# Optimization experiments

Measured on AMD Instinct MI355X. Metric: run time of the kernel, lower is better.

## Reference

```python
import jax, jax.numpy as jnp
import numpy as np

N = 50000; E = 600000; D = 128; NB = 20; L = 3; H = 64; NG = 512; ZMAX = 100
CUTOFF = 5.0

def setup_inputs() -> dict:
    key = jax.random.key(0)
    ks = jax.random.split(key, 32)
    inp = {}
    inp['at_no'] = jax.random.randint(ks[0], (N,), 0, ZMAX)
    inp['pos'] = jax.random.normal(ks[1], (N, 3), dtype=jnp.float32) * 3.0
    inp['edge_index'] = jax.random.randint(ks[2], (2, E), 0, N)
    inp['batch'] = jnp.sort(jax.random.randint(ks[3], (N,), 0, NG))
    def w(k, shape, fan_in):
        return (jax.random.normal(k, shape, dtype=jnp.float32) / np.sqrt(fan_in)).astype(jnp.float32)
    inp['emb'] = w(ks[4], (ZMAX, D), 1.0)
    # per-block filter net: rbf -> 3D
    inp['Wf'] = w(ks[5], (L, NB, 3 * D), NB); inp['bf'] = jnp.zeros((L, 3 * D), jnp.float32)
    # per-block message scalar MLP: D -> D -> 3D
    inp['Wm1'] = w(ks[6], (L, D, D), D);      inp['bm1'] = jnp.zeros((L, D), jnp.float32)
    inp['Wm2'] = w(ks[7], (L, D, 3 * D), D);  inp['bm2'] = jnp.zeros((L, 3 * D), jnp.float32)
    # per-block update: U, V channel-mixing on vectors; MLP 2D -> D -> 3D
    inp['U'] = w(ks[8], (L, D, D), D)
    inp['V'] = w(ks[9], (L, D, D), D)
    inp['Wu1'] = w(ks[10], (L, 2 * D, D), 2 * D); inp['bu1'] = jnp.zeros((L, D), jnp.float32)
    inp['Wu2'] = w(ks[11], (L, D, 3 * D), D);     inp['bu2'] = jnp.zeros((L, 3 * D), jnp.float32)
    # scalar output head: D -> H -> 1, graph sum
    inp['Wo1'] = w(ks[12], (D, H), D); inp['bo1'] = jnp.zeros((H,), jnp.float32)
    inp['Wo2'] = w(ks[13], (H, 1), H); inp['bo2'] = jnp.zeros((1,), jnp.float32)
    return inp

def _painn(at_no, pos, edge_index, batch, emb, Wf, bf, Wm1, bm1, Wm2, bm2,
           U, V, Wu1, bu1, Wu2, bu2, Wo1, bo1, Wo2, bo2):
    src, dst = edge_index[0], edge_index[1]
    vec = pos[dst] - pos[src]                       # [E,3]
    dist = jnp.sqrt(jnp.sum(vec * vec, axis=-1, keepdims=True) + 1e-12)  # [E,1]
    dirv = vec / dist                               # [E,3] (rsh l=1)
    n = jnp.arange(1, NB + 1, dtype=jnp.float32)
    rbf = jnp.sin(n * jnp.pi * dist / CUTOFF) / dist            # [E,NB] Bessel
    fcut = 0.5 * (jnp.cos(jnp.pi * dist / CUTOFF) + 1.0) * (dist < CUTOFF)  # [E,1]

    x = emb[at_no]                                  # [N,D]
    v = jnp.zeros((x.shape[0], 3, D), x.dtype)      # [N,3,D]

    for l in range(L):
        # ---- message ----
        filt = (rbf @ Wf[l] + bf[l]) * fcut                     # [E,3D]
        phi = jax.nn.silu(x @ Wm1[l] + bm1[l]) @ Wm2[l] + bm2[l]  # [N,3D]
        m = phi[src] * filt                                     # [E,3D]
        ds, dv1, dv2 = m[:, :D], m[:, D:2 * D], m[:, 2 * D:]
        dv = dv1[:, None, :] * dirv[:, :, None] + dv2[:, None, :] * v[src]  # [E,3,D]
        x = x + jax.ops.segment_sum(ds, dst, num_segments=N)
        v = v + jax.ops.segment_sum(dv, dst, num_segments=N)
        # ---- update ----
        Uv = jnp.einsum('ncd,de->nce', v, U[l])
        Vv = jnp.einsum('ncd,de->nce', v, V[l])
        Vn = jnp.sqrt(jnp.sum(Vv * Vv, axis=1) + 1e-8)          # [N,D]
        a = jax.nn.silu(jnp.concatenate([x, Vn], axis=-1) @ Wu1[l] + bu1[l]) @ Wu2[l] + bu2[l]
        avv, asv, ass = a[:, :D], a[:, D:2 * D], a[:, 2 * D:]
        x = x + ass + asv * jnp.sum(Uv * Vv, axis=1)
        v = v + avv[:, None, :] * Uv

    node_out = jax.nn.silu(x @ Wo1 + bo1) @ Wo2 + bo2           # [N,1]
    return jax.ops.segment_sum(node_out, batch, num_segments=NG)  # [NG,1]

def reference(at_no, pos, edge_index, batch, emb, Wf, bf, Wm1, bm1, Wm2, bm2,
              U, V, Wu1, bu1, Wu2, bu2, Wo1, bo1, Wo2, bo2):
    return _painn(at_no, pos, edge_index, batch, emb, Wf, bf, Wm1, bm1, Wm2, bm2,
                  U, V, Wu1, bu1, Wu2, bu2, Wo1, bo1, Wo2, bo2)
```

## Files before the change

kernel.cpp:

```cpp
#include <hip/hip_runtime.h>
#include <math.h>

#define NN 50000
#define NE 600000
#define ECAP 230000
#define DD 128
#define D3 384
#define NB_ 20
#define HH 64
#define NG_ 512
#define LSZ 180224

typedef short v8s __attribute__((ext_vector_type(8)));
typedef short v4sh __attribute__((ext_vector_type(4)));
typedef float v4f __attribute__((ext_vector_type(4)));

__device__ __forceinline__ float silu_f(float z) { return z / (1.0f + expf(-z)); }

__device__ __forceinline__ short f2bf(float f) {
  unsigned u = __float_as_uint(f);
  u += 0x7FFF + ((u >> 16) & 1);
  return (short)(u >> 16);
}
__device__ __forceinline__ float bf2f(short s) {
  return __uint_as_float(((unsigned)(unsigned short)s) << 16);
}
__device__ __forceinline__ void split2(float x, short& h, short& l) {
  h = f2bf(x);
  l = f2bf(x - bf2f(h));
}
#define SPLIT8(f0, f1, ah, al) { short h,l; \
  split2(f0.x,h,l); ah[0]=h; al[0]=l;  split2(f0.y,h,l); ah[1]=h; al[1]=l; \
  split2(f0.z,h,l); ah[2]=h; al[2]=l;  split2(f0.w,h,l); ah[3]=h; al[3]=l; \
  split2(f1.x,h,l); ah[4]=h; al[4]=l;  split2(f1.y,h,l); ah[5]=h; al[5]=l; \
  split2(f1.z,h,l); ah[6]=h; al[6]=l;  split2(f1.w,h,l); ah[7]=h; al[7]=l; }
__device__ __forceinline__ void split_store4(float4 f, short* hp, short* lp) {
  short h0,l0,h1,l1,h2,l2,h3,l3;
  split2(f.x,h0,l0); split2(f.y,h1,l1); split2(f.z,h2,l2); split2(f.w,h3,l3);
  v4sh hv = {h0,h1,h2,h3}, lv = {l0,l1,l2,l3};
  *(v4sh*)hp = hv; *(v4sh*)lp = lv;
}
#define MFMA3(acc, ah, al, bh, bl) \
  acc = __builtin_amdgcn_mfma_f32_16x16x32_bf16(ah, bh, acc, 0, 0, 0); \
  acc = __builtin_amdgcn_mfma_f32_16x16x32_bf16(al, bh, acc, 0, 0, 0); \
  acc = __builtin_amdgcn_mfma_f32_16x16x32_bf16(ah, bl, acc, 0, 0, 0);

__global__ void zero_f_kernel(float* __restrict__ p, long n) {
  long i = (long)blockIdx.x * blockDim.x + threadIdx.x;
  long s = (long)gridDim.x * blockDim.x;
  for (; i < n; i += s) p[i] = 0.0f;
}

__global__ void zero_i_kernel(int* __restrict__ p, long n) {
  long i = (long)blockIdx.x * blockDim.x + threadIdx.x;
  long s = (long)gridDim.x * blockDim.x;
  for (; i < n; i += s) p[i] = 0;
}

__global__ void init_x_kernel(const int* __restrict__ at_no, const float* __restrict__ emb,
                              float* __restrict__ x) {
  int i = blockIdx.x * blockDim.x + threadIdx.x;
  if (i >= NN * DD) return;
  x[i] = emb[at_no[i >> 7] * DD + (i & 127)];
}

__global__ void prep_w_kernel(const float* __restrict__ Wm1, const float* __restrict__ Wm2,
                              const float* __restrict__ U, const float* __restrict__ V,
                              const float* __restrict__ Wu1, const float* __restrict__ Wu2,
                              short* __restrict__ hi, short* __restrict__ lo) {
  int idx = blockIdx.x * 256 + threadIdx.x;
  if (idx >= 3 * LSZ) return;
  int l = idx / LSZ, r = idx % LSZ;
  const float* src; int K, N, nk;
  if (r < 16384)       { src = Wm1 + (size_t)l*16384; K = 128; N = 128; nk = r; }
  else if (r < 65536)  { src = Wm2 + (size_t)l*49152; K = 128; N = 384; nk = r - 16384; }
  else if (r < 81920)  { src = U   + (size_t)l*16384; K = 128; N = 128; nk = r - 65536; }
  else if (r < 98304)  { src = V   + (size_t)l*16384; K = 128; N = 128; nk = r - 81920; }
  else if (r < 131072) { src = Wu1 + (size_t)l*32768; K = 256; N = 128; nk = r - 98304; }
  else                 { src = Wu2 + (size_t)l*49152; K = 128; N = 384; nk = r - 131072; }
  int n = nk / K, k = nk - n * K;
  float xx = src[(size_t)k * N + n];
  short h = f2bf(xx);
  hi[idx] = h;
  lo[idx] = f2bf(xx - bf2f(h));
}

__global__ void hist_kernel(const int* __restrict__ ei, const float* __restrict__ pos,
                            int* __restrict__ counts) {
  int e = blockIdx.x * blockDim.x + threadIdx.x;
  if (e >= NE) return;
  int s = ei[e], d = ei[NE + e];
  float dx = pos[3*d]   - pos[3*s];
  float dy = pos[3*d+1] - pos[3*s+1];
  float dz = pos[3*d+2] - pos[3*s+2];
  float d2 = dx*dx + dy*dy + dz*dz + 1e-12f;
  if (d2 < 25.0f) atomicAdd(&counts[d], 1);
}

__global__ void scan_kernel(const int* __restrict__ counts, int* __restrict__ indptr, int n) {
  __shared__ int sm[1024];
  __shared__ int carry_s;
  if (threadIdx.x == 0) carry_s = 0;
  __syncthreads();
  for (int start = 0; start < n; start += 1024) {
    int i = start + (int)threadIdx.x;
    int val = (i < n) ? counts[i] : 0;
    sm[threadIdx.x] = val;
    __syncthreads();
    for (int off = 1; off < 1024; off <<= 1) {
      int t = (threadIdx.x >= (unsigned)off) ? sm[threadIdx.x - off] : 0;
      __syncthreads();
      sm[threadIdx.x] += t;
      __syncthreads();
    }
    int c = carry_s;
    if (i < n) indptr[i] = c + sm[threadIdx.x] - val;
    __syncthreads();
    if (threadIdx.x == 0) carry_s = c + sm[1023];
    __syncthreads();
  }
  if (threadIdx.x == 0) indptr[n] = carry_s;
}

__global__ void fill_kernel(const int* __restrict__ ei, const float* __restrict__ pos,
                            const int* __restrict__ indptr, int* __restrict__ cursor,
                            int* __restrict__ srcs, float4* __restrict__ eg1,
                            float4* __restrict__ eg2) {
  int e = blockIdx.x * blockDim.x + threadIdx.x;
  if (e >= NE) return;
  int s = ei[e], d = ei[NE + e];
  float dx = pos[3*d]   - pos[3*s];
  float dy = pos[3*d+1] - pos[3*s+1];
  float dz = pos[3*d+2] - pos[3*s+2];
  float d2 = dx*dx + dy*dy + dz*dz + 1e-12f;
  if (d2 < 25.0f) {
    int p = atomicAdd(&cursor[d], 1);
    int slot = indptr[d] + p;
    float dist = sqrtf(d2);
    float inv = 1.0f / dist;
    float wang = 0.62831853071795864769f * dist;
    float s1 = __sinf(wang), c1 = __cosf(wang);
    float fc = 0.5f * (c1 + 1.0f);
    srcs[slot] = s;
    eg1[slot] = make_float4(s1, c1, fc, fc * inv);
    eg2[slot] = make_float4(dx * inv, dy * inv, dz * inv, 0.0f);
  }
}

template<bool SILU>
__global__ void __launch_bounds__(256) mfma_gemm_kernel(
    const float* A, const short* __restrict__ Bth, const short* __restrict__ Btl,
    const float* __restrict__ bias, float* C, int M) {
  __shared__ short As2[2 * 32 * 136];
  #define ASH(r,c) As2[(r)*136 + (c)]
  #define ASL(r,c) As2[4352 + (r)*136 + (c)]
  int tid = threadIdx.x;
  long r0 = (long)blockIdx.x * 32;
  #pragma unroll
  for (int i = 0; i < 4; i++) {
    int lin = i*256 + tid;
    int r = lin >> 5, c4 = lin & 31;
    long row = r0 + r; if (row >= M) row = M - 1;
    float4 f = *(const float4*)(A + row*128 + c4*4);
    split_store4(f, &ASH(r, c4*4), &ASL(r, c4*4));
  }
  __syncthreads();
  int lane = tid & 63, wv = tid >> 6;
  int l15 = lane & 15, q = lane >> 4;
  v4f acc[2][2] = {};
  #pragma unroll
  for (int s = 0; s < 4; s++) {
    v8s ah[2], al[2];
    #pragma unroll
    for (int mt = 0; mt < 2; mt++) {
      ah[mt] = *(const v8s*)&ASH(mt*16 + l15, s*32 + q*8);
      al[mt] = *(const v8s*)&ASL(mt*16 + l15, s*32 + q*8);
    }
    #pragma unroll
    for (int nt = 0; nt < 2; nt++) {
      int n = (2*wv + nt)*16 + l15;
      v8s bh = *(const v8s*)(Bth + (long)n*128 + s*32 + q*8);
      v8s bl = *(const v8s*)(Btl + (long)n*128 + s*32 + q*8);
      #pragma unroll
      for (int mt = 0; mt < 2; mt++) { MFMA3(acc[mt][nt], ah[mt], al[mt], bh, bl); }
    }
  }
  #pragma unroll
  for (int nt = 0; nt < 2; nt++) {
    int n = (2*wv + nt)*16 + l15;
    float bb = bias[n];
    #pragma unroll
    for (int mt = 0; mt < 2; mt++)
      #pragma unroll
      for (int i = 0; i < 4; i++) {
        long row = r0 + mt*16 + q*4 + i;
        if (row < M) {
          float val = acc[mt][nt][i] + bb;
          if constexpr (SILU) val = silu_f(val);
          C[row*128 + n] = val;
        }
      }
  }
  #undef ASH
  #undef ASL
}

__global__ void __launch_bounds__(512) mfma_gemm_phi_kernel(
    const float* A, const short* __restrict__ Bth, const short* __restrict__ Btl,
    const float* __restrict__ bias,
    float* __restrict__ C0, float* __restrict__ C1, float* C2, int M) {
  __shared__ short As2[2 * 32 * 136];
  #define ASH(r,c) As2[(r)*136 + (c)]
  #define ASL(r,c) As2[4352 + (r)*136 + (c)]
  int tid = threadIdx.x;
  long r0 = (long)blockIdx.x * 32;
  #pragma unroll
  for (int i = 0; i < 2; i++) {
    int lin = i*512 + tid;
    int r = lin >> 5, c4 = lin & 31;
    long row = r0 + r; if (row >= M) row = M - 1;
    float4 f = *(const float4*)(A + row*128 + c4*4);
    split_store4(f, &ASH(r, c4*4), &ASL(r, c4*4));
  }
  __syncthreads();
  int lane = tid & 63, wv = tid >> 6;
  int l15 = lane & 15, q = lane >> 4;
  v4f acc[2][3] = {};
  #pragma unroll
  for (int s = 0; s < 4; s++) {
    v8s ah[2], al[2];
    #pragma unroll
    for (int mt = 0; mt < 2; mt++) {
      ah[mt] = *(const v8s*)&ASH(mt*16 + l15, s*32 + q*8);
      al[mt] = *(const v8s*)&ASL(mt*16 + l15, s*32 + q*8);
    }
    #pragma unroll
    for (int j = 0; j < 3; j++) {
      int n = (wv*3 + j)*16 + l15;
      v8s bh = *(const v8s*)(Bth + (long)n*128 + s*32 + q*8);
      v8s bl = *(const v8s*)(Btl + (long)n*128 + s*32 + q*8);
      #pragma unroll
      for (int mt = 0; mt < 2; mt++) { MFMA3(acc[mt][j], ah[mt], al[mt], bh, bl); }
    }
  }
  #pragma unroll
  for (int j = 0; j < 3; j++) {
    int n = (wv*3 + j)*16 + l15;
    int sl = n >> 7, col = n & 127;
    float* C = (sl == 0) ? C0 : (sl == 1) ? C1 : C2;
    float bb = bias[n];
    #pragma unroll
    for (int mt = 0; mt < 2; mt++)
      #pragma unroll
      for (int i = 0; i < 4; i++) {
        long row = r0 + mt*16 + q*4 + i;
        if (row < M) C[row*128 + col] = acc[mt][j][i] + bb;
      }
  }
  #undef ASH
  #undef ASL
}

__global__ void __launch_bounds__(512) muva_kernel(
    const float* __restrict__ phi0, const float* __restrict__ phi1,
    const float* __restrict__ phi2, const float* __restrict__ vA,
    float* __restrict__ vB, float* __restrict__ x,
    const int* __restrict__ srcs, const float4* __restrict__ eg1,
    const float4* __restrict__ eg2, const int* __restrict__ indptr,
    const float* __restrict__ Wf_l, const float* __restrict__ bf_l,
    const short* __restrict__ Uth, const short* __restrict__ Utl,
    const short* __restrict__ Vth, const short* __restrict__ Vtl,
    const short* __restrict__ W1h, const short* __restrict__ W1l, const float* __restrict__ b1,
    const short* __restrict__ W2h, const short* __restrict__ W2l, const float* __restrict__ b2) {
  __shared__ float smem[8704];
  #define VN(r,c)  smem[(r)*136 + (c)]
  #define XN(r,c)  smem[6528 + (r)*136 + (c)]
  #define CAT(r,c) smem[(r)*272 + (c)]
  #define T2(r,c)  smem[4352 + (r)*136 + (c)]
  const long NND = (long)NN*DD;
  int tid = threadIdx.x;
  long nb = (long)blockIdx.x * 16;
  {
    int g = tid >> 7, d = tid & 127;
    float wf0[NB_], wf1[NB_], wf2[NB_];
    #pragma unroll
    for (int k = 0; k < NB_; k++) {
      wf0[k] = Wf_l[k*D3 + d];
      wf1[k] = Wf_l[k*D3 + DD + d];
      wf2[k] = Wf_l[k*D3 + 2*DD + d];
    }
    float bf0 = bf_l[d], bf1 = bf_l[DD + d], bf2 = bf_l[2*DD + d];
    for (int j = 0; j < 4; j++) {
      int nr = 4*g + j;
      long n = nb + nr;
      int t = indptr[n], end = indptr[n+1];
      float xacc = 0.f, a0 = 0.f, a1 = 0.f, a2 = 0.f;
      float4 g1C = {}, g2C = {};
      float p0C = 0.f, p1C = 0.f, p2C = 0.f, w0C = 0.f, w1C = 0.f, w2C = 0.f;
      if (t < end) {
        int s0 = srcs[t]; g1C = eg1[t]; g2C = eg2[t];
        long b = (long)s0*DD + d;
        p0C = phi0[b]; p1C = phi1[b]; p2C = phi2[b];
        w0C = vA[b]; w1C = vA[NND + b]; w2C = vA[2*NND + b];
      }
      for (; t < end; t++) {
        float4 gg = g1C, dv = g2C;
        float p0 = p0C, p1 = p1C, p2 = p2C, w0 = w0C, w1 = w1C, w2 = w2C;
        if (t + 1 < end) {
          int sN = srcs[t+1]; g1C = eg1[t+1]; g2C = eg2[t+1];
          long b = (long)sN*DD + d;
          p0C = phi0[b]; p1C = phi1[b]; p2C = phi2[b];
          w0C = vA[b]; w1C = vA[NND + b]; w2C = vA[2*NND + b];
        }
        float c2 = 2.0f * gg.y;
        float rkm1 = 0.f, rk = gg.x, dot0 = 0.f, dot1 = 0.f, dot2 = 0.f;
        #pragma unroll
        for (int k = 0; k < NB_; k++) {
          dot0 = fmaf(rk, wf0[k], dot0);
          dot1 = fmaf(rk, wf1[k], dot1);
          dot2 = fmaf(rk, wf2[k], dot2);
          float rn = fmaf(c2, rk, -rkm1);
          rkm1 = rk; rk = rn;
        }
        xacc = fmaf(p0, bf0*gg.z + gg.w*dot0, xacc);
        float m1 = p1 * (bf1*gg.z + gg.w*dot1);
        float m2 = p2 * (bf2*gg.z + gg.w*dot2);
        a0 = fmaf(m1, dv.x, fmaf(m2, w0, a0));
        a1 = fmaf(m1, dv.y, fmaf(m2, w1, a1));
        a2 = fmaf(m1, dv.z, fmaf(m2, w2, a2));
      }
      long b = n*DD + d;
      XN(nr, d) = x[b] + xacc;
      VN(nr, d)      = vA[b]         + a0;
      VN(16 + nr, d) = vA[NND + b]   + a1;
      VN(32 + nr, d) = vA[2*NND + b] + a2;
    }
  }
  __syncthreads();
  int lane = tid & 63, wv = tid >> 6;
  int l15 = lane & 15, q = lane >> 4;
  int d = wv*16 + l15;
  v4f aU[3] = {}, aV[3] = {};
  #pragma unroll
  for (int s = 0; s < 4; s++) {
    long boff = (long)d*128 + s*32 + q*8;
    v8s buh = *(const v8s*)(Uth + boff);
    v8s bul = *(const v8s*)(Utl + boff);
    v8s bvh = *(const v8s*)(Vth + boff);
    v8s bvl = *(const v8s*)(Vtl + boff);
    #pragma unroll
    for (int c = 0; c < 3; c++) {
      float4 f0 = *(const float4*)&VN(c*16 + l15, s*32 + q*8);
      float4 f1 = *(const float4*)&VN(c*16 + l15, s*32 + q*8 + 4);
      v8s ah, al;
      SPLIT8(f0, f1, ah, al);
      MFMA3(aU[c], ah, al, buh, bul);
      MFMA3(aV[c], ah, al, bvh, bvl);
    }
  }
  float sreg[4], vn2[4];
  #pragma unroll
  for (int i = 0; i < 4; i++) {
    sreg[i] = aU[0][i]*aV[0][i] + aU[1][i]*aV[1][i] + aU[2][i]*aV[2][i];
    vn2[i]  = aV[0][i]*aV[0][i] + aV[1][i]*aV[1][i] + aV[2][i]*aV[2][i];
  }
  float vold[4][3];
  #pragma unroll
  for (int i = 0; i < 4; i++)
    #pragma unroll
    for (int c = 0; c < 3; c++) vold[i][c] = VN(c*16 + q*4 + i, d);
  __syncthreads();
  {
    int r = tid >> 5, c4 = tid & 31;
    *(float4*)&CAT(r, c4*4) = *(const float4*)&XN(r, c4*4);
  }
  #pragma unroll
  for (int i = 0; i < 4; i++)
    CAT(q*4 + i, 128 + d) = sqrtf(vn2[i] + 1e-8f);
  __syncthreads();
  {
    v4f acc = {};
    #pragma unroll
    for (int s = 0; s < 8; s++) {
      float4 f0 = *(const float4*)&CAT(l15, s*32 + q*8);
      float4 f1 = *(const float4*)&CAT(l15, s*32 + q*8 + 4);
      v8s ah, al;
      SPLIT8(f0, f1, ah, al);
      v8s bh = *(const v8s*)(W1h + (long)d*256 + s*32 + q*8);
      v8s bl = *(const v8s*)(W1l + (long)d*256 + s*32 + q*8);
      MFMA3(acc, ah, al, bh, bl);
    }
    float bb = b1[d];
    #pragma unroll
    for (int i = 0; i < 4; i++)
      T2(q*4 + i, d) = silu_f(acc[i] + bb);
  }
  __syncthreads();
  {
    v4f acc[3] = {};
    #pragma unroll
    for (int s = 0; s < 4; s++) {
      float4 f0 = *(const float4*)&T2(l15, s*32 + q*8);
      float4 f1 = *(const float4*)&T2(l15, s*32 + q*8 + 4);
      v8s ah, al;
      SPLIT8(f0, f1, ah, al);
      #pragma unroll
      for (int g = 0; g < 3; g++) {
        int n = g*128 + d;
        v8s bh = *(const v8s*)(W2h + (long)n*128 + s*32 + q*8);
        v8s bl = *(const v8s*)(W2l + (long)n*128 + s*32 + q*8);
        MFMA3(acc[g], ah, al, bh, bl);
      }
    }
    float bavv = b2[d], basv = b2[128 + d], bass = b2[256 + d];
    #pragma unroll
    for (int i = 0; i < 4; i++) {
      int lr = q*4 + i;
      long row = nb + lr;
      float avv = acc[0][i] + bavv;
      float asv = acc[1][i] + basv;
      float ass = acc[2][i] + bass;
      x[row*DD + d] = CAT(lr, d) + ass + asv * sreg[i];
      #pragma unroll
      for (int c = 0; c < 3; c++)
        vB[(long)c*NND + row*DD + d] = fmaf(avv, aU[c][i], vold[i][c]);
    }
  }
  #undef VN
  #undef XN
  #undef CAT
  #undef T2
}

__global__ void __launch_bounds__(256) out_kernel(
    const float* __restrict__ x, const float* __restrict__ Wo1,
    const float* __restrict__ bo1, const float* __restrict__ Wo2,
    const float* __restrict__ bo2, const int* __restrict__ batch,
    float* __restrict__ out) {
  __shared__ float xs[4][132];
  int tid = threadIdx.x;
  long n0 = (long)blockIdx.x * 4;
  if (tid < 128) {
    int r = tid >> 5, c4 = tid & 31;
    *(float4*)&xs[r][c4*4] = *(const float4*)(x + (n0 + r)*128 + c4*4);
  }
  __syncthreads();
  int wv = tid >> 6, t = tid & 63;
  float acc = bo1[t];
  #pragma unroll 16
  for (int k = 0; k < DD; k++) acc = fmaf(xs[wv][k], Wo1[k*HH + t], acc);
  float val = silu_f(acc) * Wo2[t];
  #pragma unroll
  for (int off = 32; off > 0; off >>= 1) val += __shfl_down(val, off);
  if (t == 0) atomicAdd(&out[batch[n0 + wv]], val + bo2[0]);
}

extern "C" void kernel_launch(void* const* d_in, const int* in_sizes, int n_in,
                              void* d_out, int out_size, void* d_ws, size_t ws_size,
                              hipStream_t stream) {
  const int*   at_no = (const int*)d_in[0];
  const float* pos   = (const float*)d_in[1];
  const int*   ei    = (const int*)d_in[2];
  const int*   batch = (const int*)d_in[3];
  const float* emb   = (const float*)d_in[4];
  const float* Wf    = (const float*)d_in[5];
  const float* bfp   = (const float*)d_in[6];
  const float* Wm1   = (const float*)d_in[7];
  const float* bm1   = (const float*)d_in[8];
  const float* Wm2   = (const float*)d_in[9];
  const float* bm2   = (const float*)d_in[10];
  const float* U     = (const float*)d_in[11];
  const float* V     = (const float*)d_in[12];
  const float* Wu1   = (const float*)d_in[13];
  const float* bu1   = (const float*)d_in[14];
  const float* Wu2   = (const float*)d_in[15];
  const float* bu2   = (const float*)d_in[16];
  const float* Wo1   = (const float*)d_in[17];
  const float* bo1   = (const float*)d_in[18];
  const float* Wo2   = (const float*)d_in[19];
  const float* bo2   = (const float*)d_in[20];
  float* out = (float*)d_out;

  char* w = (char*)d_ws;
  auto alloc = [&](size_t bytes) -> void* {
    void* p = (void*)w;
    w += (bytes + 255) & ~(size_t)255;
    return p;
  };
  float*  x      = (float*)alloc(sizeof(float)*(size_t)NN*DD);
  float*  v_a    = (float*)alloc(sizeof(float)*(size_t)NN*D3);
  float*  v_b    = (float*)alloc(sizeof(float)*(size_t)NN*D3);
  float*  t1     = (float*)alloc(sizeof(float)*(size_t)NN*DD);
  float*  phiS   = (float*)alloc(sizeof(float)*(size_t)NN*DD);
  float*  phi0   = (float*)alloc(sizeof(float)*(size_t)NN*DD);
  short*  wbh    = (short*)alloc(sizeof(short)*(size_t)3*LSZ);
  short*  wbl    = (short*)alloc(sizeof(short)*(size_t)3*LSZ);
  int*    srcs   = (int*)alloc(sizeof(int)*(size_t)ECAP);
  float4* eg1    = (float4*)alloc(sizeof(float4)*(size_t)ECAP);
  float4* eg2    = (float4*)alloc(sizeof(float4)*(size_t)ECAP);
  int*    indptr = (int*)alloc(sizeof(int)*((size_t)NN+1));
  int*    counts = (int*)alloc(sizeof(int)*(size_t)NN);

  if ((size_t)(w - (char*)d_ws) > ws_size) {
    zero_f_kernel<<<2, 256, 0, stream>>>(out, NG_);
    return;
  }

  zero_f_kernel<<<2048, 256, 0, stream>>>(v_a, (long)NN*D3);
  zero_f_kernel<<<2, 256, 0, stream>>>(out, NG_);
  zero_i_kernel<<<64, 256, 0, stream>>>(counts, NN);
  init_x_kernel<<<(NN*DD + 255)/256, 256, 0, stream>>>(at_no, emb, x);
  prep_w_kernel<<<(3*LSZ + 255)/256, 256, 0, stream>>>(Wm1, Wm2, U, V, Wu1, Wu2, wbh, wbl);
  hist_kernel<<<(NE + 255)/256, 256, 0, stream>>>(ei, pos, counts);
  scan_kernel<<<1, 1024, 0, stream>>>(counts, indptr, NN);
  zero_i_kernel<<<64, 256, 0, stream>>>(counts, NN);
  fill_kernel<<<(NE + 255)/256, 256, 0, stream>>>(ei, pos, indptr, counts, srcs, eg1, eg2);

  const int MB = (NN + 31) / 32;
  float* vcur = v_a;
  float* vnext = v_b;
  for (int l = 0; l < 3; l++) {
    const float* Wf_l  = Wf  + (size_t)l*NB_*D3;
    const float* bf_l  = bfp + (size_t)l*D3;
    const float* bm1_l = bm1 + (size_t)l*DD;
    const float* bm2_l = bm2 + (size_t)l*D3;
    const float* bu1_l = bu1 + (size_t)l*DD;
    const float* bu2_l = bu2 + (size_t)l*D3;
    const short* Lh = wbh + (size_t)l*LSZ;
    const short* Ll = wbl + (size_t)l*LSZ;
    const short* Wm1h = Lh,          *Wm1L = Ll;
    const short* Wm2h = Lh + 16384,  *Wm2L = Ll + 16384;
    const short* Uh   = Lh + 65536,  *UL   = Ll + 65536;
    const short* Vh   = Lh + 81920,  *VL   = Ll + 81920;
    const short* Wu1h = Lh + 98304,  *Wu1L = Ll + 98304;
    const short* Wu2h = Lh + 131072, *Wu2L = Ll + 131072;

    mfma_gemm_kernel<true><<<MB, 256, 0, stream>>>(x, Wm1h, Wm1L, bm1_l, t1, NN);
    mfma_gemm_phi_kernel<<<MB, 512, 0, stream>>>(t1, Wm2h, Wm2L, bm2_l, phi0, phiS, t1, NN);
    muva_kernel<<<NN/16, 512, 0, stream>>>(phi0, phiS, t1, vcur, vnext, x,
                                           srcs, eg1, eg2, indptr, Wf_l, bf_l,
                                           Uh, UL, Vh, VL,
                                           Wu1h, Wu1L, bu1_l, Wu2h, Wu2L, bu2_l);

    float* tmp = vcur; vcur = vnext; vnext = tmp;
  }

  out_kernel<<<NN/4, 256, 0, stream>>>(x, Wo1, bo1, Wo2, bo2, batch, out);

  (void)in_sizes; (void)n_in; (void)out_size; (void)ws_size;
}
```

Measured before the change: 1.477 ms.

## Split Chebyshev sine recurrence into four chains, widen GEMM blocks, pad LDS

The per-edge Bessel sine recurrence now runs as four independent stride-4 Chebyshev chains using cos(4θ) multipliers, with separate partial dot accumulators. This shortens the serial FMA dependency chain in the edge loop of the message kernel. The first MLP GEMM now uses 512 threads with one N-tile per wave instead of two, and the LDS row strides in the update kernel are padded to cut bank conflicts. The stride-4 recurrence changes rounding slightly and uses more registers.

```diff
diff --git a/kernel.cpp b/kernel.cpp
--- a/kernel.cpp
+++ b/kernel.cpp
@@ -148,7 +148,7 @@
 }
 
 template<bool SILU>
-__global__ void __launch_bounds__(256) mfma_gemm_kernel(
+__global__ void __launch_bounds__(512) mfma_gemm_kernel(
     const float* A, const short* __restrict__ Bth, const short* __restrict__ Btl,
     const float* __restrict__ bias, float* C, int M) {
   __shared__ short As2[2 * 32 * 136];
@@ -157,8 +157,8 @@
   int tid = threadIdx.x;
   long r0 = (long)blockIdx.x * 32;
   #pragma unroll
-  for (int i = 0; i < 4; i++) {
-    int lin = i*256 + tid;
+  for (int i = 0; i < 2; i++) {
+    int lin = i*512 + tid;
     int r = lin >> 5, c4 = lin & 31;
     long row = r0 + r; if (row >= M) row = M - 1;
     float4 f = *(const float4*)(A + row*128 + c4*4);
@@ -167,40 +167,31 @@
   __syncthreads();
   int lane = tid & 63, wv = tid >> 6;
   int l15 = lane & 15, q = lane >> 4;
-  v4f acc[2][2] = {};
+  int n = wv*16 + l15;
+  v4f acc[2] = {};
   #pragma unroll
   for (int s = 0; s < 4; s++) {
-    v8s ah[2], al[2];
+    v8s bh = *(const v8s*)(Bth + (long)n*128 + s*32 + q*8);
+    v8s bl = *(const v8s*)(Btl + (long)n*128 + s*32 + q*8);
     #pragma unroll
     for (int mt = 0; mt < 2; mt++) {
-      ah[mt] = *(const v8s*)&ASH(mt*16 + l15, s*32 + q*8);
-      al[mt] = *(const v8s*)&ASL(mt*16 + l15, s*32 + q*8);
-    }
-    #pragma unroll
-    for (int nt = 0; nt < 2; nt++) {
-      int n = (2*wv + nt)*16 + l15;
-      v8s bh = *(const v8s*)(Bth + (long)n*128 + s*32 + q*8);
-      v8s bl = *(const v8s*)(Btl + (long)n*128 + s*32 + q*8);
-      #pragma unroll
-      for (int mt = 0; mt < 2; mt++) { MFMA3(acc[mt][nt], ah[mt], al[mt], bh, bl); }
-    }
-  }
-  #pragma unroll
-  for (int nt = 0; nt < 2; nt++) {
-    int n = (2*wv + nt)*16 + l15;
-    float bb = bias[n];
-    #pragma unroll
-    for (int mt = 0; mt < 2; mt++)
-      #pragma unroll
-      for (int i = 0; i < 4; i++) {
-        long row = r0 + mt*16 + q*4 + i;
-        if (row < M) {
-          float val = acc[mt][nt][i] + bb;
-          if constexpr (SILU) val = silu_f(val);
-          C[row*128 + n] = val;
-        }
+      v8s ah = *(const v8s*)&ASH(mt*16 + l15, s*32 + q*8);
+      v8s al = *(const v8s*)&ASL(mt*16 + l15, s*32 + q*8);
+      MFMA3(acc[mt], ah, al, bh, bl);
+    }
+  }
+  float bb = bias[n];
+  #pragma unroll
+  for (int mt = 0; mt < 2; mt++)
+    #pragma unroll
+    for (int i = 0; i < 4; i++) {
+      long row = r0 + mt*16 + q*4 + i;
+      if (row < M) {
+        float val = acc[mt][i] + bb;
+        if constexpr (SILU) val = silu_f(val);
+        C[row*128 + n] = val;
       }
-  }
+    }
   #undef ASH
   #undef ASL
 }
@@ -272,11 +263,11 @@
     const short* __restrict__ Vth, const short* __restrict__ Vtl,
     const short* __restrict__ W1h, const short* __restrict__ W1l, const float* __restrict__ b1,
     const short* __restrict__ W2h, const short* __restrict__ W2l, const float* __restrict__ b2) {
-  __shared__ float smem[8704];
-  #define VN(r,c)  smem[(r)*136 + (c)]
-  #define XN(r,c)  smem[6528 + (r)*136 + (c)]
-  #define CAT(r,c) smem[(r)*272 + (c)]
-  #define T2(r,c)  smem[4352 + (r)*136 + (c)]
+  __shared__ float smem[8896];
+  #define VN(r,c)  smem[(r)*140 + (c)]
+  #define XN(r,c)  smem[6720 + (r)*136 + (c)]
+  #define CAT(r,c) smem[(r)*276 + (c)]
+  #define T2(r,c)  smem[4416 + (r)*140 + (c)]
   const long NND = (long)NN*DD;
   int tid = threadIdx.x;
   long nb = (long)blockIdx.x * 16;
@@ -312,19 +303,48 @@
           p0C = phi0[b]; p1C = phi1[b]; p2C = phi2[b];
           w0C = vA[b]; w1C = vA[NND + b]; w2C = vA[2*NND + b];
         }
-        float c2 = 2.0f * gg.y;
-        float rkm1 = 0.f, rk = gg.x, dot0 = 0.f, dot1 = 0.f, dot2 = 0.f;
+        float s1 = gg.x, c1 = gg.y, fc = gg.z, base = gg.w;
+        float c2v = 2.0f * c1;
+        float cc2 = fmaf(c2v, c1, -1.0f);
+        float s2  = c2v * s1;
+        float s3  = s1 * fmaf(2.0f, cc2, 1.0f);
+        float s4  = 2.0f * s2 * cc2;
+        float C8  = 2.0f * fmaf(2.0f*cc2, cc2, -1.0f);
+        float ra0 = s1, rb0 = -s3;
+        float ra1 = s2, rb1 = -s2;
+        float ra2 = s3, rb2 = -s1;
+        float ra3 = s4, rb3 = 0.f;
+        float d0p0=0,d0p1=0,d0p2=0,d0p3=0;
+        float d1p0=0,d1p1=0,d1p2=0,d1p3=0;
+        float d2p0=0,d2p1=0,d2p2=0,d2p3=0;
         #pragma unroll
-        for (int k = 0; k < NB_; k++) {
-          dot0 = fmaf(rk, wf0[k], dot0);
-          dot1 = fmaf(rk, wf1[k], dot1);
-          dot2 = fmaf(rk, wf2[k], dot2);
-          float rn = fmaf(c2, rk, -rkm1);
-          rkm1 = rk; rk = rn;
+        for (int jj = 0; jj < 5; jj++) {
+          int k0 = 4*jj;
+          d0p0 = fmaf(ra0, wf0[k0],   d0p0);
+          d1p0 = fmaf(ra0, wf1[k0],   d1p0);
+          d2p0 = fmaf(ra0, wf2[k0],   d2p0);
+          d0p1 = fmaf(ra1, wf0[k0+1], d0p1);
+          d1p1 = fmaf(ra1, wf1[k0+1], d1p1);
+          d2p1 = fmaf(ra1, wf2[k0+1], d2p1);
+          d0p2 = fmaf(ra2, wf0[k0+2], d0p2);
+          d1p2 = fmaf(ra2, wf1[k0+2], d1p2);
+          d2p2 = fmaf(ra2, wf2[k0+2], d2p2);
+          d0p3 = fmaf(ra3, wf0[k0+3], d0p3);
+          d1p3 = fmaf(ra3, wf1[k0+3], d1p3);
+          d2p3 = fmaf(ra3, wf2[k0+3], d2p3);
+          if (jj < 4) {
+            float n0 = fmaf(C8, ra0, -rb0); rb0 = ra0; ra0 = n0;
+            float n1 = fmaf(C8, ra1, -rb1); rb1 = ra1; ra1 = n1;
+            float n2 = fmaf(C8, ra2, -rb2); rb2 = ra2; ra2 = n2;
+            float n3 = fmaf(C8, ra3, -rb3); rb3 = ra3; ra3 = n3;
+          }
         }
-        xacc = fmaf(p0, bf0*gg.z + gg.w*dot0, xacc);
-        float m1 = p1 * (bf1*gg.z + gg.w*dot1);
-        float m2 = p2 * (bf2*gg.z + gg.w*dot2);
+        float dot0 = (d0p0 + d0p1) + (d0p2 + d0p3);
+        float dot1 = (d1p0 + d1p1) + (d1p2 + d1p3);
+        float dot2 = (d2p0 + d2p1) + (d2p2 + d2p3);
+        xacc = fmaf(p0, fmaf(bf0, fc, base*dot0), xacc);
+        float m1 = p1 * fmaf(bf1, fc, base*dot1);
+        float m2 = p2 * fmaf(bf2, fc, base*dot2);
         a0 = fmaf(m1, dv.x, fmaf(m2, w0, a0));
         a1 = fmaf(m1, dv.y, fmaf(m2, w1, a1));
         a2 = fmaf(m1, dv.z, fmaf(m2, w2, a2));
@@ -535,7 +555,7 @@
     const short* Wu1h = Lh + 98304,  *Wu1L = Ll + 98304;
     const short* Wu2h = Lh + 131072, *Wu2L = Ll + 131072;
 
-    mfma_gemm_kernel<true><<<MB, 256, 0, stream>>>(x, Wm1h, Wm1L, bm1_l, t1, NN);
+    mfma_gemm_kernel<true><<<MB, 512, 0, stream>>>(x, Wm1h, Wm1L, bm1_l, t1, NN);
     mfma_gemm_phi_kernel<<<MB, 512, 0, stream>>>(t1, Wm2h, Wm2L, bm2_l, phi0, phiS, t1, NN);
     muva_kernel<<<NN/16, 512, 0, stream>>>(phi0, phiS, t1, vcur, vnext, x,
                                            srcs, eg1, eg2, indptr, Wf_l, bf_l,
```

Measured after the change: 1.804 ms. 1.22x slower.
